# Kernel optimization log

Hardware: AMD Instinct MI355X
Metric: run time of the kernel (lower is better)

The kernel has to match this reference:

```python
import jax, jax.numpy as jnp
import numpy as np

H = 768      # hidden_size
R = 64       # lora_dim
E = 8        # n_experts
B, S = 8, 2048


def setup_inputs() -> dict:
    key = jax.random.key(0)
    ks = jax.random.split(key, 10)
    s_in = 1.0 / np.sqrt(H)
    s_r = 1.0 / np.sqrt(R)
    return {
        "x": jax.random.normal(ks[0], (B, S, H), dtype=jnp.float32),
        "enc_w": jax.random.uniform(ks[1], (H, R), jnp.float32, -s_in, s_in),
        "enc_b": jax.random.uniform(ks[2], (R,), jnp.float32, -s_in, s_in),
        "sw_w": jax.random.uniform(ks[3], (R, E), jnp.float32, -s_r, s_r),
        "sw_b": jax.random.uniform(ks[4], (E,), jnp.float32, -s_r, s_r),
        "w1": jax.random.uniform(ks[5], (E, H, R), jnp.float32, -s_in, s_in),
        "b1": jax.random.uniform(ks[6], (E, R), jnp.float32, -s_in, s_in),
        "w2": jax.random.uniform(ks[7], (E, R, H), jnp.float32, -s_r, s_r),
        "b2": jax.random.uniform(ks[8], (E, H), jnp.float32, -s_r, s_r),
    }


def reference(x, enc_w, enc_b, sw_w, sw_b, w1, b1, w2, b2):
    b, s, d = x.shape
    xt = x.reshape(-1, d)                                  # [T, H]
    # router: encoder -> switch -> softmax -> top-1
    x_enc = xt @ enc_w + enc_b                             # [T, R]
    route_prob = jax.nn.softmax(x_enc @ sw_w + sw_b, axis=-1)  # [T, E]
    route_prob_max = jnp.max(route_prob, axis=-1)          # [T]
    routes = jnp.argmax(route_prob, axis=-1)               # [T]
    onehot = jax.nn.one_hot(routes, E, dtype=xt.dtype)     # [T, E]
    # dense dispatch: per-(token, expert) LoRA bottleneck; masked combine
    h = jnp.einsum('td,edr->ter', xt, w1) + b1[None]       # [T, E, R]
    h = jax.nn.gelu(h, approximate=False)
    h = h * onehot[..., None]                              # zero non-routed
    out = jnp.einsum('ter,erd->td', h, w2) + onehot @ b2   # [T, H]
    out = out * route_prob_max[:, None]
    return out.reshape(b, s, d)
```

## Files before the change

### kernel.cpp

```cpp
#include <hip/hip_runtime.h>
#include <math.h>

#define HDIM 768
#define RDIM 64
#define NEXP 8
#define NTOK 16384

typedef _Float16 half8 __attribute__((ext_vector_type(8)));
typedef float float4_t __attribute__((ext_vector_type(4)));

__device__ __forceinline__ float gelu_exact(float v) {
    return 0.5f * v * (1.0f + erff(v * 0.70710678118654752440f));
}

__global__ __launch_bounds__(256) void prep_kernel(
    const float* __restrict__ w1, const float* __restrict__ w2,
    const float* __restrict__ enc_w,
    _Float16* __restrict__ w1t, _Float16* __restrict__ w2t,
    _Float16* __restrict__ enc_hi, _Float16* __restrict__ enc_lo)
{
    const int wid = blockIdx.x * 4 + (threadIdx.x >> 6);
    const int lane = threadIdx.x & 63;
    if (wid < 768) {
        const int e = wid / 96, k0 = (wid % 96) * 8;
        half8 o;
        #pragma unroll
        for (int j = 0; j < 8; j++)
            o[j] = (_Float16)w1[((size_t)(e * HDIM + k0 + j)) * RDIM + lane];
        *(half8*)(w1t + ((size_t)(e * RDIM + lane)) * HDIM + k0) = o;
    } else if (wid < 1536) {
        const int id = wid - 768;
        const int e = id / 96, rem = id % 96;
        const int n = (rem >> 3) * 64 + lane, k0 = (rem & 7) * 8;
        half8 o;
        #pragma unroll
        for (int j = 0; j < 8; j++)
            o[j] = (_Float16)w2[((size_t)(e * RDIM + k0 + j)) * HDIM + n];
        *(half8*)(w2t + ((size_t)(e * HDIM + n)) * RDIM + k0) = o;
    } else if (wid < 1632) {
        const int k0 = (wid - 1536) * 8;
        half8 hi, lo;
        #pragma unroll
        for (int j = 0; j < 8; j++) {
            float v = enc_w[(size_t)(k0 + j) * RDIM + lane];
            _Float16 h = (_Float16)v;
            hi[j] = h;
            lo[j] = (_Float16)(v - (float)h);
        }
        *(half8*)(enc_hi + (size_t)lane * HDIM + k0) = hi;
        *(half8*)(enc_lo + (size_t)lane * HDIM + k0) = lo;
    }
}

__global__ __launch_bounds__(256) void router_kernel(
    const float* __restrict__ x,
    const _Float16* __restrict__ enc_hi, const _Float16* __restrict__ enc_lo,
    const float* __restrict__ enc_b, const float* __restrict__ sw_w,
    const float* __restrict__ sw_b, float* __restrict__ pmax,
    int* __restrict__ counts, int* __restrict__ lists)
{
    __shared__ __align__(16) float part[4][16][68];
    __shared__ __align__(16) float sws[512];
    __shared__ int lcnt[NEXP], gbase[NEXP];

    const int tid = threadIdx.x;
    const int tok0 = blockIdx.x * 16;
    const int wv = tid >> 6, lane = tid & 63;
    const int q = lane >> 4, c = lane & 15;

    if (tid < 128) ((float4*)sws)[tid] = ((const float4*)sw_w)[tid];
    if (tid < NEXP) lcnt[tid] = 0;

    const float* xrow = x + (size_t)(tok0 + c) * HDIM + wv * 192;
    const _Float16* ebase_hi = enc_hi + (size_t)c * HDIM + wv * 192 + q * 8;
    const _Float16* ebase_lo = enc_lo + (size_t)c * HDIM + wv * 192 + q * 8;

    float4_t acc[4] = {{0,0,0,0},{0,0,0,0},{0,0,0,0},{0,0,0,0}};
    #pragma unroll
    for (int it = 0; it < 6; it++) {
        const int k0 = it * 32;
        float4 u0 = *(const float4*)(xrow + k0 + q * 8);
        float4 u1 = *(const float4*)(xrow + k0 + q * 8 + 4);
        float u[8] = {u0.x, u0.y, u0.z, u0.w, u1.x, u1.y, u1.z, u1.w};
        half8 ah, al;
        #pragma unroll
        for (int j = 0; j < 8; j++) {
            _Float16 hv = (_Float16)u[j];
            ah[j] = hv;
            al[j] = (_Float16)(u[j] - (float)hv);
        }
        #pragma unroll
        for (int nf = 0; nf < 4; nf++) {
            half8 bh = *(const half8*)(ebase_hi + (size_t)nf * 16 * HDIM + k0);
            half8 bl = *(const half8*)(ebase_lo + (size_t)nf * 16 * HDIM + k0);
            acc[nf] = __builtin_amdgcn_mfma_f32_16x16x32_f16(ah, bh, acc[nf], 0, 0, 0);
            acc[nf] = __builtin_amdgcn_mfma_f32_16x16x32_f16(ah, bl, acc[nf], 0, 0, 0);
            acc[nf] = __builtin_amdgcn_mfma_f32_16x16x32_f16(al, bh, acc[nf], 0, 0, 0);
        }
    }

    #pragma unroll
    for (int nf = 0; nf < 4; nf++)
        #pragma unroll
        for (int i = 0; i < 4; i++)
            part[wv][q * 4 + i][nf * 16 + c] = acc[nf][i];
    __syncthreads();

    #pragma unroll
    for (int j = 0; j < 4; j++) {
        const int idx = tid + 256 * j;
        const int row = idx >> 6, r = idx & 63;
        float v = part[0][row][r] + part[1][row][r] + part[2][row][r]
                + part[3][row][r] + enc_b[r];
        part[0][row][r] = v;
    }
    __syncthreads();

    int am_s = -1, lp_s = 0;
    if (tid < 128) {
        const int e = tid & 7;
        const int t = tid >> 3;
        float logit = sw_b[e];
        #pragma unroll 16
        for (int r = 0; r < RDIM; r++)
            logit += part[0][t][r] * sws[r * NEXP + e];
        float m = logit; int am = e;
        #pragma unroll
        for (int d = 4; d >= 1; d >>= 1) {
            float om = __shfl_xor(m, d, 8);
            int oam  = __shfl_xor(am, d, 8);
            if (om > m || (om == m && oam < am)) { m = om; am = oam; }
        }
        float s = expf(logit - m);
        #pragma unroll
        for (int d = 1; d <= 4; d <<= 1) s += __shfl_xor(s, d, 8);
        if (e == 0) {
            pmax[tok0 + t] = 1.0f / s;
            am_s = am;
            lp_s = atomicAdd(&lcnt[am], 1);
        }
    }
    __syncthreads();
    if (tid < NEXP) gbase[tid] = atomicAdd(&counts[tid * 32], lcnt[tid]);
    __syncthreads();
    if (am_s >= 0)
        lists[am_s * NTOK + gbase[am_s] + lp_s] = tok0 + (tid >> 3);
}

__global__ __launch_bounds__(256) void mm1_kernel(
    const float* __restrict__ x, const _Float16* __restrict__ w1t,
    const float* __restrict__ b1, const int* __restrict__ counts,
    const int* __restrict__ lists, _Float16* __restrict__ h)
{
    __shared__ __align__(16) float part[4][16][68];

    const int e = blockIdx.x;
    const int cnt = counts[e * 32];
    const int tid = threadIdx.x;
    const int wv = tid >> 6, lane = tid & 63;
    const int q = lane >> 4, c = lane & 15;

    for (int st = blockIdx.y; st * 16 < cnt; st += gridDim.y) {
        const int base = st * 16;
        const int nt = cnt - base;
        const int tA = lists[e * NTOK + base + min(c, nt - 1)];
        const float* xrow = x + (size_t)tA * HDIM + wv * 192;
        const _Float16* wbase = w1t + ((size_t)(e * RDIM + c)) * HDIM + wv * 192 + q * 8;

        float4_t acc[4] = {{0,0,0,0},{0,0,0,0},{0,0,0,0},{0,0,0,0}};
        #pragma unroll
        for (int it = 0; it < 6; it++) {
            const int k0 = it * 32;
            float4 u0 = *(const float4*)(xrow + k0 + q * 8);
            float4 u1 = *(const float4*)(xrow + k0 + q * 8 + 4);
            half8 a;
            a[0] = (_Float16)u0.x; a[1] = (_Float16)u0.y;
            a[2] = (_Float16)u0.z; a[3] = (_Float16)u0.w;
            a[4] = (_Float16)u1.x; a[5] = (_Float16)u1.y;
            a[6] = (_Float16)u1.z; a[7] = (_Float16)u1.w;
            #pragma unroll
            for (int nf = 0; nf < 4; nf++) {
                half8 b = *(const half8*)(wbase + (size_t)nf * 16 * HDIM + k0);
                acc[nf] = __builtin_amdgcn_mfma_f32_16x16x32_f16(a, b, acc[nf], 0, 0, 0);
            }
        }

        #pragma unroll
        for (int nf = 0; nf < 4; nf++)
            #pragma unroll
            for (int i = 0; i < 4; i++)
                part[wv][q * 4 + i][nf * 16 + c] = acc[nf][i];
        __syncthreads();

        #pragma unroll
        for (int j = 0; j < 4; j++) {
            const int idx = tid + 256 * j;
            const int row = idx >> 6, r = idx & 63;
            if (row < nt) {
                const int tok = lists[e * NTOK + base + row];
                float v = part[0][row][r] + part[1][row][r] + part[2][row][r]
                        + part[3][row][r] + b1[e * RDIM + r];
                h[(size_t)tok * RDIM + r] = (_Float16)gelu_exact(v);
            }
        }
        __syncthreads();
    }
}

__global__ __launch_bounds__(256) void mm2_kernel(
    const _Float16* __restrict__ h, const _Float16* __restrict__ w2t,
    const float* __restrict__ b2, const float* __restrict__ pmax,
    const int* __restrict__ counts, const int* __restrict__ lists,
    float* __restrict__ out)
{
    const int e = blockIdx.x;
    const int cnt = counts[e * 32];
    const int wv = threadIdx.x >> 6, lane = threadIdx.x & 63;
    const int q = lane >> 4, c = lane & 15;

    const int task = blockIdx.y * 4 + wv;
    const int nch = task % 3;
    const int sidx = task / 3;

    for (int st = sidx; st * 16 < cnt; st += 128) {
        const int base = st * 16;
        const int nt = cnt - base;
        const int tA = lists[e * NTOK + base + min(c, nt - 1)];
        half8 a0 = *(const half8*)(h + (size_t)tA * RDIM + q * 8);
        half8 a1 = *(const half8*)(h + (size_t)tA * RDIM + 32 + q * 8);

        int tokv[4]; float pm[4]; bool ok[4];
        #pragma unroll
        for (int i = 0; i < 4; i++) {
            const int row = q * 4 + i;
            ok[i] = row < nt;
            tokv[i] = lists[e * NTOK + base + min(row, nt - 1)];
            pm[i] = pmax[tokv[i]];
        }

        #pragma unroll 4
        for (int nf = 0; nf < 16; nf++) {
            const int n = nch * 256 + nf * 16 + c;
            const _Float16* wrow = w2t + ((size_t)(e * HDIM + n)) * RDIM;
            half8 b0 = *(const half8*)(wrow + q * 8);
            half8 b1v = *(const half8*)(wrow + 32 + q * 8);
            float4_t acc = {0, 0, 0, 0};
            acc = __builtin_amdgcn_mfma_f32_16x16x32_f16(a0, b0, acc, 0, 0, 0);
            acc = __builtin_amdgcn_mfma_f32_16x16x32_f16(a1, b1v, acc, 0, 0, 0);
            const float b2v = b2[e * HDIM + n];
            #pragma unroll
            for (int i = 0; i < 4; i++) {
                if (ok[i])
                    out[(size_t)tokv[i] * HDIM + n] = (acc[i] + b2v) * pm[i];
            }
        }
    }
}

extern "C" void kernel_launch(void* const* d_in, const int* in_sizes, int n_in,
                              void* d_out, int out_size, void* d_ws, size_t ws_size,
                              hipStream_t stream) {
    const float* x     = (const float*)d_in[0];
    const float* enc_w = (const float*)d_in[1];
    const float* enc_b = (const float*)d_in[2];
    const float* sw_w  = (const float*)d_in[3];
    const float* sw_b  = (const float*)d_in[4];
    const float* w1    = (const float*)d_in[5];
    const float* b1    = (const float*)d_in[6];
    const float* w2    = (const float*)d_in[7];
    const float* b2    = (const float*)d_in[8];
    float* out = (float*)d_out;

    char* p = (char*)d_ws;
    int*      counts = (int*)p;
    float*    pmax   = (float*)(p + 1024);
    int*      lists  = (int*)(p + 1024 + 65536);
    _Float16* enc_hi = (_Float16*)(p + 590848);
    _Float16* enc_lo = (_Float16*)(p + 590848 + 98304);
    _Float16* w1t    = (_Float16*)(p + 590848 + 196608);
    _Float16* w2t    = (_Float16*)(p + 590848 + 196608 + 786432);
    _Float16* h      = (_Float16*)(p + 590848 + 196608 + 1572864);

    hipMemsetAsync(d_ws, 0, 1024, stream);

    hipLaunchKernelGGL(prep_kernel, dim3(408), dim3(256), 0, stream,
                       w1, w2, enc_w, w1t, w2t, enc_hi, enc_lo);
    hipLaunchKernelGGL(router_kernel, dim3(NTOK / 16), dim3(256), 0, stream,
                       x, enc_hi, enc_lo, enc_b, sw_w, sw_b, pmax, counts, lists);
    hipLaunchKernelGGL(mm1_kernel, dim3(NEXP, 128), dim3(256), 0, stream,
                       x, w1t, b1, counts, lists, h);
    hipLaunchKernelGGL(mm2_kernel, dim3(NEXP, 96), dim3(256), 0, stream,
                       h, w2t, b2, pmax, counts, lists, out);
}
```

Before: 206.1 us.

## Fold router encoder and switch weights into one HxE projection

Since the router is linear up to the softmax, enc_w and sw_w are pre-multiplied in the prep kernel into a single 768x8 matrix plus a combined bias. The router then computes 8 logits per token with FP32 FMAs from shared memory, replacing the split-precision 3x MFMA encoder GEMM. This removes most of the router's arithmetic and the hi/lo weight buffers. In exchange, reassociating the sums can flip argmax on near-tied tokens. The change also prefetches all x loads up front in mm1 and adds occupancy hints to launch_bounds.

Result: faster. 195.2 us (-5.3%).

```diff
diff --git a/kernel.cpp b/kernel.cpp
--- a/kernel.cpp
+++ b/kernel.cpp
@@ -15,9 +15,10 @@
 
 __global__ __launch_bounds__(256) void prep_kernel(
     const float* __restrict__ w1, const float* __restrict__ w2,
-    const float* __restrict__ enc_w,
+    const float* __restrict__ enc_w, const float* __restrict__ enc_b,
+    const float* __restrict__ sw_w, const float* __restrict__ sw_b,
     _Float16* __restrict__ w1t, _Float16* __restrict__ w2t,
-    _Float16* __restrict__ enc_hi, _Float16* __restrict__ enc_lo)
+    float* __restrict__ wrt, float* __restrict__ brr)
 {
     const int wid = blockIdx.x * 4 + (threadIdx.x >> 6);
     const int lane = threadIdx.x & 63;
@@ -38,116 +39,89 @@
             o[j] = (_Float16)w2[((size_t)(e * RDIM + k0 + j)) * HDIM + n];
         *(half8*)(w2t + ((size_t)(e * HDIM + n)) * RDIM + k0) = o;
     } else if (wid < 1632) {
-        const int k0 = (wid - 1536) * 8;
-        half8 hi, lo;
-        #pragma unroll
-        for (int j = 0; j < 8; j++) {
-            float v = enc_w[(size_t)(k0 + j) * RDIM + lane];
-            _Float16 h = (_Float16)v;
-            hi[j] = h;
-            lo[j] = (_Float16)(v - (float)h);
-        }
-        *(half8*)(enc_hi + (size_t)lane * HDIM + k0) = hi;
-        *(half8*)(enc_lo + (size_t)lane * HDIM + k0) = lo;
-    }
-}
-
-__global__ __launch_bounds__(256) void router_kernel(
-    const float* __restrict__ x,
-    const _Float16* __restrict__ enc_hi, const _Float16* __restrict__ enc_lo,
-    const float* __restrict__ enc_b, const float* __restrict__ sw_w,
-    const float* __restrict__ sw_b, float* __restrict__ pmax,
-    int* __restrict__ counts, int* __restrict__ lists)
-{
-    __shared__ __align__(16) float part[4][16][68];
-    __shared__ __align__(16) float sws[512];
-    __shared__ int lcnt[NEXP], gbase[NEXP];
-
-    const int tid = threadIdx.x;
-    const int tok0 = blockIdx.x * 16;
-    const int wv = tid >> 6, lane = tid & 63;
-    const int q = lane >> 4, c = lane & 15;
-
-    if (tid < 128) ((float4*)sws)[tid] = ((const float4*)sw_w)[tid];
-    if (tid < NEXP) lcnt[tid] = 0;
-
-    const float* xrow = x + (size_t)(tok0 + c) * HDIM + wv * 192;
-    const _Float16* ebase_hi = enc_hi + (size_t)c * HDIM + wv * 192 + q * 8;
-    const _Float16* ebase_lo = enc_lo + (size_t)c * HDIM + wv * 192 + q * 8;
-
-    float4_t acc[4] = {{0,0,0,0},{0,0,0,0},{0,0,0,0},{0,0,0,0}};
-    #pragma unroll
-    for (int it = 0; it < 6; it++) {
-        const int k0 = it * 32;
-        float4 u0 = *(const float4*)(xrow + k0 + q * 8);
-        float4 u1 = *(const float4*)(xrow + k0 + q * 8 + 4);
-        float u[8] = {u0.x, u0.y, u0.z, u0.w, u1.x, u1.y, u1.z, u1.w};
-        half8 ah, al;
-        #pragma unroll
-        for (int j = 0; j < 8; j++) {
-            _Float16 hv = (_Float16)u[j];
-            ah[j] = hv;
-            al[j] = (_Float16)(u[j] - (float)hv);
-        }
-        #pragma unroll
-        for (int nf = 0; nf < 4; nf++) {
-            half8 bh = *(const half8*)(ebase_hi + (size_t)nf * 16 * HDIM + k0);
-            half8 bl = *(const half8*)(ebase_lo + (size_t)nf * 16 * HDIM + k0);
-            acc[nf] = __builtin_amdgcn_mfma_f32_16x16x32_f16(ah, bh, acc[nf], 0, 0, 0);
-            acc[nf] = __builtin_amdgcn_mfma_f32_16x16x32_f16(ah, bl, acc[nf], 0, 0, 0);
-            acc[nf] = __builtin_amdgcn_mfma_f32_16x16x32_f16(al, bh, acc[nf], 0, 0, 0);
-        }
-    }
-
-    #pragma unroll
-    for (int nf = 0; nf < 4; nf++)
-        #pragma unroll
-        for (int i = 0; i < 4; i++)
-            part[wv][q * 4 + i][nf * 16 + c] = acc[nf][i];
-    __syncthreads();
-
-    #pragma unroll
-    for (int j = 0; j < 4; j++) {
-        const int idx = tid + 256 * j;
-        const int row = idx >> 6, r = idx & 63;
-        float v = part[0][row][r] + part[1][row][r] + part[2][row][r]
-                + part[3][row][r] + enc_b[r];
-        part[0][row][r] = v;
-    }
-    __syncthreads();
-
-    int am_s = -1, lp_s = 0;
-    if (tid < 128) {
-        const int e = tid & 7;
-        const int t = tid >> 3;
-        float logit = sw_b[e];
+        const int k = (wid - 1536) * 8 + (lane >> 3);
+        const int e = lane & 7;
+        float s = 0.0f;
         #pragma unroll 16
         for (int r = 0; r < RDIM; r++)
-            logit += part[0][t][r] * sws[r * NEXP + e];
-        float m = logit; int am = e;
-        #pragma unroll
-        for (int d = 4; d >= 1; d >>= 1) {
-            float om = __shfl_xor(m, d, 8);
-            int oam  = __shfl_xor(am, d, 8);
-            if (om > m || (om == m && oam < am)) { m = om; am = oam; }
-        }
-        float s = expf(logit - m);
-        #pragma unroll
-        for (int d = 1; d <= 4; d <<= 1) s += __shfl_xor(s, d, 8);
-        if (e == 0) {
-            pmax[tok0 + t] = 1.0f / s;
-            am_s = am;
-            lp_s = atomicAdd(&lcnt[am], 1);
-        }
+            s += enc_w[(size_t)k * RDIM + r] * sw_w[r * NEXP + e];
+        wrt[e * HDIM + k] = s;
+    } else if (wid == 1632) {
+        if (lane < NEXP) {
+            float s = sw_b[lane];
+            #pragma unroll 16
+            for (int r = 0; r < RDIM; r++)
+                s += enc_b[r] * sw_w[r * NEXP + lane];
+            brr[lane] = s;
+        }
+    }
+}
+
+__global__ __launch_bounds__(256, 4) void router_kernel(
+    const float* __restrict__ x, const float* __restrict__ wrt,
+    const float* __restrict__ brr, float* __restrict__ pmax,
+    int* __restrict__ counts, int* __restrict__ lists)
+{
+    __shared__ __align__(16) float wrl[NEXP][772];
+    __shared__ int lcnt[NEXP], gbase[NEXP];
+
+    const int tid = threadIdx.x;
+    #pragma unroll
+    for (int i0 = 0; i0 < 6; i0++) {
+        const int i = tid + i0 * 256;
+        const int e = i / 192, k4 = (i % 192) * 4;
+        *(float4*)&wrl[e][k4] = *(const float4*)(wrt + e * HDIM + k4);
+    }
+    if (tid < NEXP) lcnt[tid] = 0;
+    __syncthreads();
+
+    const int wv = tid >> 6, lane = tid & 63;
+    const int e = lane & 7, tslot = lane >> 3;
+    const int tok = blockIdx.x * 32 + wv * 8 + tslot;
+    const float* xrow = x + (size_t)tok * HDIM;
+
+    float4_t acc4 = {0.0f, 0.0f, 0.0f, 0.0f};
+    for (int k0 = 0; k0 < HDIM; k0 += 64) {
+        float4 xv[16];
+        #pragma unroll
+        for (int u = 0; u < 16; u++)
+            xv[u] = *(const float4*)(xrow + k0 + u * 4);
+        #pragma unroll
+        for (int u = 0; u < 16; u++) {
+            const float4 w4 = *(const float4*)(&wrl[e][k0 + u * 4]);
+            acc4[0] = fmaf(xv[u].x, w4.x, acc4[0]);
+            acc4[1] = fmaf(xv[u].y, w4.y, acc4[1]);
+            acc4[2] = fmaf(xv[u].z, w4.z, acc4[2]);
+            acc4[3] = fmaf(xv[u].w, w4.w, acc4[3]);
+        }
+    }
+    const float logit = (acc4[0] + acc4[1]) + (acc4[2] + acc4[3]) + brr[e];
+
+    float m = logit; int am = e;
+    #pragma unroll
+    for (int d = 4; d >= 1; d >>= 1) {
+        float om = __shfl_xor(m, d, 8);
+        int oam  = __shfl_xor(am, d, 8);
+        if (om > m || (om == m && oam < am)) { m = om; am = oam; }
+    }
+    float s = expf(logit - m);
+    #pragma unroll
+    for (int d = 1; d <= 4; d <<= 1) s += __shfl_xor(s, d, 8);
+
+    int am_s = -1, lp_s = 0;
+    if (e == 0) {
+        pmax[tok] = 1.0f / s;
+        am_s = am;
+        lp_s = atomicAdd(&lcnt[am], 1);
     }
     __syncthreads();
     if (tid < NEXP) gbase[tid] = atomicAdd(&counts[tid * 32], lcnt[tid]);
     __syncthreads();
     if (am_s >= 0)
-        lists[am_s * NTOK + gbase[am_s] + lp_s] = tok0 + (tid >> 3);
-}
-
-__global__ __launch_bounds__(256) void mm1_kernel(
+        lists[am_s * NTOK + gbase[am_s] + lp_s] = tok;
+}
+
+__global__ __launch_bounds__(256, 4) void mm1_kernel(
     const float* __restrict__ x, const _Float16* __restrict__ w1t,
     const float* __restrict__ b1, const int* __restrict__ counts,
     const int* __restrict__ lists, _Float16* __restrict__ h)
@@ -167,17 +141,22 @@
         const float* xrow = x + (size_t)tA * HDIM + wv * 192;
         const _Float16* wbase = w1t + ((size_t)(e * RDIM + c)) * HDIM + wv * 192 + q * 8;
 
+        float4 xv[12];
+        #pragma unroll
+        for (int it = 0; it < 6; it++) {
+            xv[2 * it]     = *(const float4*)(xrow + it * 32 + q * 8);
+            xv[2 * it + 1] = *(const float4*)(xrow + it * 32 + q * 8 + 4);
+        }
+
         float4_t acc[4] = {{0,0,0,0},{0,0,0,0},{0,0,0,0},{0,0,0,0}};
         #pragma unroll
         for (int it = 0; it < 6; it++) {
             const int k0 = it * 32;
-            float4 u0 = *(const float4*)(xrow + k0 + q * 8);
-            float4 u1 = *(const float4*)(xrow + k0 + q * 8 + 4);
             half8 a;
-            a[0] = (_Float16)u0.x; a[1] = (_Float16)u0.y;
-            a[2] = (_Float16)u0.z; a[3] = (_Float16)u0.w;
-            a[4] = (_Float16)u1.x; a[5] = (_Float16)u1.y;
-            a[6] = (_Float16)u1.z; a[7] = (_Float16)u1.w;
+            a[0] = (_Float16)xv[2*it].x;   a[1] = (_Float16)xv[2*it].y;
+            a[2] = (_Float16)xv[2*it].z;   a[3] = (_Float16)xv[2*it].w;
+            a[4] = (_Float16)xv[2*it+1].x; a[5] = (_Float16)xv[2*it+1].y;
+            a[6] = (_Float16)xv[2*it+1].z; a[7] = (_Float16)xv[2*it+1].w;
             #pragma unroll
             for (int nf = 0; nf < 4; nf++) {
                 half8 b = *(const half8*)(wbase + (size_t)nf * 16 * HDIM + k0);
@@ -207,7 +186,7 @@
     }
 }
 
-__global__ __launch_bounds__(256) void mm2_kernel(
+__global__ __launch_bounds__(256, 3) void mm2_kernel(
     const _Float16* __restrict__ h, const _Float16* __restrict__ w2t,
     const float* __restrict__ b2, const float* __restrict__ pmax,
     const int* __restrict__ counts, const int* __restrict__ lists,
@@ -274,19 +253,19 @@
     char* p = (char*)d_ws;
     int*      counts = (int*)p;
     float*    pmax   = (float*)(p + 1024);
-    int*      lists  = (int*)(p + 1024 + 65536);
-    _Float16* enc_hi = (_Float16*)(p + 590848);
-    _Float16* enc_lo = (_Float16*)(p + 590848 + 98304);
-    _Float16* w1t    = (_Float16*)(p + 590848 + 196608);
-    _Float16* w2t    = (_Float16*)(p + 590848 + 196608 + 786432);
-    _Float16* h      = (_Float16*)(p + 590848 + 196608 + 1572864);
+    int*      lists  = (int*)(p + 66560);
+    float*    wrt    = (float*)(p + 590848);
+    float*    brr    = (float*)(p + 615424);
+    _Float16* w1t    = (_Float16*)(p + 615680);
+    _Float16* w2t    = (_Float16*)(p + 1402112);
+    _Float16* h      = (_Float16*)(p + 2188544);
 
     hipMemsetAsync(d_ws, 0, 1024, stream);
 
-    hipLaunchKernelGGL(prep_kernel, dim3(408), dim3(256), 0, stream,
-                       w1, w2, enc_w, w1t, w2t, enc_hi, enc_lo);
-    hipLaunchKernelGGL(router_kernel, dim3(NTOK / 16), dim3(256), 0, stream,
-                       x, enc_hi, enc_lo, enc_b, sw_w, sw_b, pmax, counts, lists);
+    hipLaunchKernelGGL(prep_kernel, dim3(409), dim3(256), 0, stream,
+                       w1, w2, enc_w, enc_b, sw_w, sw_b, w1t, w2t, wrt, brr);
+    hipLaunchKernelGGL(router_kernel, dim3(NTOK / 32), dim3(256), 0, stream,
+                       x, wrt, brr, pmax, counts, lists);
     hipLaunchKernelGGL(mm1_kernel, dim3(NEXP, 128), dim3(256), 0, stream,
                        x, w1t, b1, counts, lists, h);
     hipLaunchKernelGGL(mm2_kernel, dim3(NEXP, 96), dim3(256), 0, stream,
```
